# Kernel optimization log

Measured on AMD Instinct MI355X. Metric: run time of the kernel, lower is better.

## Reference

```python
import jax, jax.numpy as jnp
import numpy as np

N_NODES = 10000
N_EDGES = 160000
C = 16        # num_feature_channels
C2 = 8        # output channels per irrep per head (C/2)
HID = 64      # radial_network_hidden_units
NH = 2        # num_attention_heads
NG = 16       # graphs in batch
F_IN = 64     # num_features
F_OUT = 32    # number_of_output_features
HEAD_TYPES = ("normal", "inverse")  # invariant_dictionary
IRREP_SLICES = ((0, 1), (1, 4), (4, 9))  # l=0,1,2 blocks of the SH dim


def _sph_harm(r):
    """Component-normalized real spherical harmonics l=0..2 for unit vectors r [E,3] -> [E,9]."""
    x, y, z = r[:, 0], r[:, 1], r[:, 2]
    c3 = 1.7320508   # sqrt(3)
    c15 = 3.8729833  # sqrt(15)
    l0 = jnp.ones_like(x)[:, None]
    l1 = c3 * r
    l2 = jnp.stack([
        c15 * x * y,
        c15 * y * z,
        1.1180340 * (2.0 * z * z - x * x - y * y),  # sqrt(5)/2
        c15 * x * z,
        1.9364917 * (x * x - y * y),                 # sqrt(15)/2
    ], axis=-1)
    return jnp.concatenate([l0, l1, l2], axis=-1)


def setup_inputs() -> dict:
    key = jax.random.key(0)
    ks = jax.random.split(key, 16)
    node_features = jax.random.normal(ks[0], (N_NODES, F_IN), jnp.float32)
    pos = jax.random.normal(ks[1], (N_NODES, 3), jnp.float32)
    src = jax.random.randint(ks[2], (N_EDGES,), 0, N_NODES)
    off = jax.random.randint(ks[3], (N_EDGES,), 1, N_NODES)  # avoid self-loops (d=0)
    tgt = (src + off) % N_NODES
    edge_index = jnp.stack([src, tgt], axis=0)
    batch = jnp.sort(jax.random.randint(ks[4], (N_NODES,), 0, NG))
    s = lambda k, shape, fan: (jax.random.normal(k, shape, jnp.float32) / np.sqrt(fan)).astype(jnp.float32)
    return dict(
        node_features=node_features, pos=pos,
        W_embed=s(ks[5], (F_IN, C), F_IN), b_embed=jnp.zeros((C,), jnp.float32),
        Wq=s(ks[6], (NH, C, C), C), Wk=s(ks[7], (NH, C, C), C),
        W1=s(ks[8], (NH, 1, HID), 1), b1=jnp.zeros((NH, HID), jnp.float32),
        Wa=s(ks[9], (NH, HID), HID), Wv=s(ks[10], (NH, HID, C * 3), HID),
        Wo=s(ks[11], (NH, 3, C, C2), C),
        Wproj=s(ks[12], (NH * C2, F_OUT), NH * C2), bproj=jnp.zeros((F_OUT,), jnp.float32),
        edge_index=edge_index, batch=batch,
    )


def _forward(node_features, pos, W_embed, b_embed, Wq, Wk, W1, b1, Wa, Wv, Wo,
             Wproj, bproj, edge_index, batch):
    src, tgt = edge_index[0], edge_index[1]
    rel = pos[tgt] - pos[src]                       # [E,3]
    dist = jnp.linalg.norm(rel, axis=-1, keepdims=True)  # [E,1]
    rhat = rel / dist
    Y = _sph_harm(rhat)                             # [E,9]
    x = node_features @ W_embed + b_embed          # [N,C] scalar (0e) features
    xs = x[src]                                     # [E,C]
    inv_sqrt_c = 1.0 / np.sqrt(C)
    head_outs = []
    for h in range(NH):
        d_feat = dist if HEAD_TYPES[h] == "normal" else dist ** -2  # [E,1]
        hid = jax.nn.relu(d_feat @ W1[h] + b1[h])   # [E,HID] radial network
        att_bias = hid @ Wa[h]                      # [E]
        wv = (hid @ Wv[h]).reshape(-1, C, 3)        # [E,C,3] per-(channel,l) radial weights
        q = x @ Wq[h]
        k = x @ Wk[h]
        logit = jnp.sum(q[tgt] * k[src], axis=-1) * inv_sqrt_c + att_bias  # [E]
        # segment softmax over incoming edges of each target node
        m = jax.ops.segment_max(logit, tgt, num_segments=N_NODES)
        e = jnp.exp(logit - m[tgt])
        z = jax.ops.segment_sum(e, tgt, num_segments=N_NODES)
        alpha = e / z[tgt]                          # [E]
        # expand per-l weights to per-m: dims (1,3,5)
        wv_m = jnp.repeat(wv, np.array([1, 3, 5]), axis=2, total_repeat_length=9)  # [E,C,9]
        msg = (alpha[:, None, None] * wv_m) * xs[:, :, None] * Y[:, None, :]       # [E,C,9]
        node_out = jax.ops.segment_sum(msg, tgt, num_segments=N_NODES)             # [N,C,9]
        parts = [jnp.einsum('ncm,co->nom', node_out[:, :, s0:s1], Wo[h, li]).reshape(N_NODES, -1)
                 for li, (s0, s1) in enumerate(IRREP_SLICES)]
        head_outs.append(jnp.concatenate(parts, axis=-1))  # [N, C2*9]
    feat = jnp.concatenate(head_outs, axis=-1)              # [N, NH*C2*9]
    pooled = jax.ops.segment_sum(feat, batch, num_segments=NG)  # [NG, NH*C2*9]
    # equivariant Linear -> F_OUT x 0e: only scalar (l=0) components map to scalars
    blk = C2 * 9
    scal = jnp.concatenate([pooled[:, h * blk: h * blk + C2] for h in range(NH)], axis=-1)  # [NG, NH*C2]
    return scal @ Wproj + bproj                             # [NG, F_OUT]


def reference(node_features, pos, W_embed, b_embed, Wq, Wk, W1, b1, Wa, Wv, Wo,
              Wproj, bproj, edge_index, batch):
    return _forward(node_features, pos, W_embed, b_embed, Wq, Wk, W1, b1, Wa, Wv,
                    Wo, Wproj, bproj, edge_index, batch)
```

## Files before the change

### kernel.cpp

```cpp
#include <hip/hip_runtime.h>
#include <math.h>

#define NN 10000
#define NE 160000
#define CAP 96

__device__ __forceinline__ unsigned bf16pack2(float a, float b) {
    unsigned ua = __float_as_uint(a);
    unsigned ub = __float_as_uint(b);
    ua = ua + 0x7fffu + ((ua >> 16) & 1u);
    ub = ub + 0x7fffu + ((ub >> 16) & 1u);
    return (ua >> 16) | (ub & 0xffff0000u);
}

__global__ __launch_bounds__(256) void k_xqk(const float* __restrict__ nf,
        const float* __restrict__ We, const float* __restrict__ be,
        const float* __restrict__ Wq, const float* __restrict__ Wk,
        float* __restrict__ x, float* __restrict__ q, float* __restrict__ k,
        int* __restrict__ zeroReg) {
    int t = threadIdx.x;
    int gid = blockIdx.x * 256 + t;
    if (gid < 10256) zeroReg[gid] = 0;
    __shared__ float sWe[64 * 16];
    __shared__ float sWq[2 * 16 * 16];
    __shared__ float sWk[2 * 16 * 16];
    __shared__ float sNF[16 * 64];
    __shared__ float sX[16 * 16];
    for (int i = t; i < 1024; i += 256) sWe[i] = We[i];
    for (int i = t; i < 512; i += 256) { sWq[i] = Wq[i]; sWk[i] = Wk[i]; }
    int nodeBase = blockIdx.x * 16;
    for (int i = t; i < 1024; i += 256) {
        int n = nodeBase + (i >> 6);
        sNF[i] = (n < NN) ? nf[n * 64 + (i & 63)] : 0.0f;
    }
    __syncthreads();
    int ln = t >> 4, c = t & 15;
    int n = nodeBase + ln;
    float acc = be[c];
    #pragma unroll 16
    for (int j = 0; j < 64; ++j) acc = fmaf(sNF[ln * 64 + j], sWe[j * 16 + c], acc);
    sX[ln * 16 + c] = acc;
    __syncthreads();
    if (n < NN) {
        x[n * 16 + c] = acc;
        #pragma unroll
        for (int h = 0; h < 2; ++h) {
            float aq = 0.0f, ak = 0.0f;
            #pragma unroll
            for (int j = 0; j < 16; ++j) {
                float xv = sX[ln * 16 + j];
                aq = fmaf(xv, sWq[(h * 16 + j) * 16 + c], aq);
                ak = fmaf(xv, sWk[(h * 16 + j) * 16 + c], ak);
            }
            q[(n * 2 + h) * 16 + c] = aq;
            k[(n * 2 + h) * 16 + c] = ak;
        }
    }
}

__global__ __launch_bounds__(256) void k_prep(const float* __restrict__ W1,
        const float* __restrict__ b1, const float* __restrict__ Wa,
        const float* __restrict__ Wv,
        float* __restrict__ sTau, float* __restrict__ gT) {
    __shared__ float sW[128], sB[128], sA[128], sT[128];
    __shared__ float sV[2048];
    __shared__ int sRank[128];
    int t = threadIdx.x;
    if (t < 128) { sW[t] = W1[t]; sB[t] = b1[t]; sA[t] = Wa[t]; }
    for (int i = t; i < 2048; i += 256) {
        int h = i >> 10, j = (i >> 4) & 63, c = i & 15;
        sV[i] = Wv[(h * 64 + j) * 48 + 3 * c];
    }
    __syncthreads();
    if (t < 128) {
        float w = sW[t], b = sB[t];
        sT[t] = (w != 0.0f) ? (-b / w) : ((b > 0.0f) ? -INFINITY : INFINITY);
    }
    __syncthreads();
    if (t < 128) {
        int h = t >> 6, j = t & 63;
        float tau = sT[t];
        int r = 0;
        for (int jj = 0; jj < 64; ++jj) {
            float o = sT[h * 64 + jj];
            r += (o < tau) || (o == tau && jj < j);
        }
        sRank[t] = r;
        if (blockIdx.x == 0) sTau[h * 64 + r] = tau;
    }
    __syncthreads();
    int idx = blockIdx.x * 256 + t;
    if (idx < 2210) {
        int h = idx / 1105;
        int rem = idx - h * 1105;
        int k = rem / 17;
        int c = rem - k * 17;
        float A = 0.0f, B = 0.0f;
        for (int j = 0; j < 64; ++j) {
            int jj = h * 64 + j;
            float w = sW[jj], b = sB[jj];
            bool posSlope = (w >= 0.0f);
            int r = sRank[jj];
            bool active = posSlope ? (r < k) : (r >= k);
            if (active) {
                float v = (c < 16) ? sV[h * 1024 + j * 16 + c] : sA[jj];
                A = fmaf(w, v, A);
                B = fmaf(b, v, B);
            }
        }
        float* row = gT + (h * 65 + k) * 36;
        if (c < 16) { row[c] = A; row[20 + c] = B; }
        else        { row[16] = A; row[17] = B; }
    }
}

__global__ __launch_bounds__(256) void k_edge(const float* __restrict__ pos,
        const int* __restrict__ ei,
        const float* __restrict__ q, const float* __restrict__ k,
        const float* __restrict__ sTau, const float* __restrict__ gT,
        const float* __restrict__ Wo,
        const float* __restrict__ x, int* __restrict__ deg,
        float* __restrict__ lgp, uint4* __restrict__ gb) {
    int e = blockIdx.x * 256 + threadIdx.x;
    if (e >= NE) return;
    int s = ei[e], t = ei[NE + e];
    int p = atomicAdd(&deg[t], 1);
    bool ok = (p < CAP);
    size_t slot = (size_t)t * CAP + p;
    float dx = pos[t * 3 + 0] - pos[s * 3 + 0];
    float dy = pos[t * 3 + 1] - pos[s * 3 + 1];
    float dz = pos[t * 3 + 2] - pos[s * 3 + 2];
    float d = sqrtf(dx * dx + dy * dy + dz * dz);
    float fh[2] = { d, 1.0f / (d * d) };
    const float4* xp = (const float4*)(x + (size_t)s * 16);
    float4 xs0 = xp[0], xs1 = xp[1], xs2 = xp[2], xs3 = xp[3];
    float xf[16] = { xs0.x, xs0.y, xs0.z, xs0.w, xs1.x, xs1.y, xs1.z, xs1.w,
                     xs2.x, xs2.y, xs2.z, xs2.w, xs3.x, xs3.y, xs3.z, xs3.w };
    float L2v[2];
    #pragma unroll
    for (int h = 0; h < 2; ++h) {
        const float4* qt = (const float4*)(q + (size_t)t * 32 + h * 16);
        const float4* ks = (const float4*)(k + (size_t)s * 32 + h * 16);
        float4 a0 = qt[0], a1 = qt[1], a2 = qt[2], a3 = qt[3];
        float4 b0 = ks[0], c1 = ks[1], c2 = ks[2], c3 = ks[3];
        float dot = a0.x * b0.x + a0.y * b0.y + a0.z * b0.z + a0.w * b0.w
                  + a1.x * c1.x + a1.y * c1.y + a1.z * c1.z + a1.w * c1.w
                  + a2.x * c2.x + a2.y * c2.y + a2.z * c2.z + a2.w * c2.w
                  + a3.x * c3.x + a3.y * c3.y + a3.z * c3.z + a3.w * c3.w;
        float f = fh[h];
        const float* tb = sTau + h * 64;
        int kk = 0;
        #pragma unroll
        for (int step = 64; step >= 1; step >>= 1) {
            int mid = kk + step;
            if (mid <= 64 && tb[mid - 1] <= f) kk = mid;
        }
        const float* row = gT + (h * 65 + kk) * 36;
        float4 A0 = *(const float4*)(row + 0);
        float4 A1 = *(const float4*)(row + 4);
        float4 A2 = *(const float4*)(row + 8);
        float4 A3 = *(const float4*)(row + 12);
        float2 AB = *(const float2*)(row + 16);
        float4 B0 = *(const float4*)(row + 20);
        float4 B1 = *(const float4*)(row + 24);
        float4 B2 = *(const float4*)(row + 28);
        float4 B3 = *(const float4*)(row + 32);
        L2v[h] = fmaf(dot, 0.25f, fmaf(AB.x, f, AB.y));
        float acc[16] = {
            fmaf(A0.x, f, B0.x), fmaf(A0.y, f, B0.y), fmaf(A0.z, f, B0.z), fmaf(A0.w, f, B0.w),
            fmaf(A1.x, f, B1.x), fmaf(A1.y, f, B1.y), fmaf(A1.z, f, B1.z), fmaf(A1.w, f, B1.w),
            fmaf(A2.x, f, B2.x), fmaf(A2.y, f, B2.y), fmaf(A2.z, f, B2.z), fmaf(A2.w, f, B2.w),
            fmaf(A3.x, f, B3.x), fmaf(A3.y, f, B3.y), fmaf(A3.z, f, B3.z), fmaf(A3.w, f, B3.w) };
        float g[8] = {0,0,0,0,0,0,0,0};
        const float* wob = Wo + h * 384;
        #pragma unroll
        for (int c = 0; c < 16; ++c) {
            float axc = acc[c] * xf[c];
            #pragma unroll
            for (int o = 0; o < 8; ++o) g[o] = fmaf(axc, wob[c * 8 + o], g[o]);
        }
        if (ok) {
            gb[slot * 2 + h] = make_uint4(bf16pack2(g[0], g[1]), bf16pack2(g[2], g[3]),
                                          bf16pack2(g[4], g[5]), bf16pack2(g[6], g[7]));
        }
    }
    if (ok) *(float2*)(lgp + slot * 2) = make_float2(L2v[0], L2v[1]);
}

__global__ __launch_bounds__(256) void k_gather(const int* __restrict__ deg,
        const float* __restrict__ lgp, const unsigned* __restrict__ gb,
        float* __restrict__ feat) {
    int t0 = threadIdx.x;
    int wv = t0 >> 6;
    int lane = t0 & 63;
    int pid = blockIdx.x * 4 + wv;
    int n = pid >> 1, h = pid & 1;
    int dg = min(deg[n], CAP);
    int g = lane >> 2, p = lane & 3;
    float m = -INFINITY, z = 0.0f, u0 = 0.0f, u1 = 0.0f;
    const float* lgb = lgp + (size_t)n * (CAP * 2) + h;
    const unsigned* gbb = gb + (size_t)n * (CAP * 8) + h * 4 + p;
    for (int i = g; i < dg; i += 16) {
        float L = lgb[i * 2];
        unsigned wbits = gbb[(size_t)i * 8];
        float ga = __uint_as_float(wbits << 16);
        float gbv = __uint_as_float(wbits & 0xffff0000u);
        float nm = fmaxf(m, L);
        float sc = (m > -INFINITY) ? __expf(m - nm) : 0.0f;
        float w  = __expf(L - nm);
        u0 = fmaf(u0, sc, w * ga);
        u1 = fmaf(u1, sc, w * gbv);
        z  = fmaf(z, sc, w);
        m = nm;
    }
    #pragma unroll
    for (int off = 4; off <= 32; off <<= 1) {
        float mo = __shfl_xor(m, off, 64);
        float zo = __shfl_xor(z, off, 64);
        float a0o = __shfl_xor(u0, off, 64);
        float a1o = __shfl_xor(u1, off, 64);
        float nm = fmaxf(m, mo);
        float a = (m  > -INFINITY) ? __expf(m  - nm) : 0.0f;
        float b = (mo > -INFINITY) ? __expf(mo - nm) : 0.0f;
        u0 = u0 * a + a0o * b;
        u1 = u1 * a + a1o * b;
        z  = z * a + zo * b;
        m = nm;
    }
    if (lane < 4) {
        float inv = (z > 0.0f) ? 1.0f / z : 0.0f;
        *(float2*)(feat + n * 16 + h * 8 + p * 2) = make_float2(u0 * inv, u1 * inv);
    }
}

__global__ __launch_bounds__(256) void k_pool(const float* __restrict__ feat,
        const int* __restrict__ batch, float* __restrict__ pooled) {
    __shared__ float sP[256];
    int t = threadIdx.x;
    sP[t] = 0.0f;
    __syncthreads();
    int tid = blockIdx.x * 256 + t;
    int c = tid & 15, seg = tid >> 4;
    int n0 = seg * 16, n1 = min(n0 + 16, NN);
    float run = 0.0f;
    int curg = -1;
    for (int n = n0; n < n1; ++n) {
        int gg = batch[n];
        if (gg != curg) {
            if (curg >= 0) atomicAdd(&sP[curg * 16 + c], run);
            run = 0.0f; curg = gg;
        }
        run += feat[n * 16 + c];
    }
    if (curg >= 0) atomicAdd(&sP[curg * 16 + c], run);
    __syncthreads();
    atomicAdd(&pooled[t], sP[t]);
}

__global__ __launch_bounds__(512) void k_final(const float* __restrict__ pooled,
        const float* __restrict__ Wproj, const float* __restrict__ bproj,
        float* __restrict__ out) {
    int t = threadIdx.x;
    int g = t >> 5, fo = t & 31;
    float acc = bproj[fo];
    #pragma unroll
    for (int j = 0; j < 16; ++j) acc = fmaf(pooled[g * 16 + j], Wproj[j * 32 + fo], acc);
    out[g * 32 + fo] = acc;
}

extern "C" void kernel_launch(void* const* d_in, const int* in_sizes, int n_in,
                              void* d_out, int out_size, void* d_ws, size_t ws_size,
                              hipStream_t stream) {
    const float* nf    = (const float*)d_in[0];
    const float* pos   = (const float*)d_in[1];
    const float* We    = (const float*)d_in[2];
    const float* be    = (const float*)d_in[3];
    const float* Wq    = (const float*)d_in[4];
    const float* Wk    = (const float*)d_in[5];
    const float* W1    = (const float*)d_in[6];
    const float* b1    = (const float*)d_in[7];
    const float* Wa    = (const float*)d_in[8];
    const float* Wv    = (const float*)d_in[9];
    const float* Wo    = (const float*)d_in[10];
    const float* Wproj = (const float*)d_in[11];
    const float* bproj = (const float*)d_in[12];
    const int*   ei    = (const int*)d_in[13];
    const int*   batch = (const int*)d_in[14];
    float* out = (float*)d_out;
    (void)in_sizes; (void)n_in; (void)out_size; (void)ws_size;

    float* ws     = (float*)d_ws;
    float* x      = ws;
    float* q      = x + 160000;
    float* k      = q + 320000;
    float* feat   = k + 320000;
    float* pooled = feat + 160000;
    int*   deg    = (int*)(pooled + 256);
    float* sTau   = (float*)(deg + 10000);
    float* gT     = sTau + 128;
    float* lgp    = gT + 4680;
    unsigned* gbu = (unsigned*)(lgp + (size_t)NN * CAP * 2);

    hipLaunchKernelGGL(k_xqk,    dim3(625),  dim3(256), 0, stream, nf, We, be, Wq, Wk, x, q, k, (int*)pooled);
    hipLaunchKernelGGL(k_prep,   dim3(9),    dim3(256), 0, stream, W1, b1, Wa, Wv, sTau, gT);
    hipLaunchKernelGGL(k_edge,   dim3(625),  dim3(256), 0, stream, pos, ei, q, k, sTau, gT, Wo, x, deg, lgp, (uint4*)gbu);
    hipLaunchKernelGGL(k_gather, dim3(5000), dim3(256), 0, stream, deg, lgp, gbu, feat);
    hipLaunchKernelGGL(k_pool,   dim3(40),   dim3(256), 0, stream, feat, batch, pooled);
    hipLaunchKernelGGL(k_final,  dim3(1),    dim3(512), 0, stream, pooled, Wproj, bproj, out);
}
```

Baseline: 136.5 us.

## Fuse prep into xqk and gather/pool/final into one kernel with atomic tickets

Runs the radial-table prep as extra blocks of the node-embedding kernel, and merges gather, pooling and the final projection into one kernel. The last 40 blocks to finish (by atomic ticket) spin until all blocks are done, then pool, and the very last block computes the output. This cuts six launches to three, removing launch gaps and inter-kernel idle time. The cost is a spin-wait and device-scope fences, which depend on the ticketed blocks being resident while earlier blocks finish.

Result: slower. 520.9 us (+281.6%).

```diff
diff --git a/kernel.cpp b/kernel.cpp
--- a/kernel.cpp
+++ b/kernel.cpp
@@ -16,11 +16,66 @@
 __global__ __launch_bounds__(256) void k_xqk(const float* __restrict__ nf,
         const float* __restrict__ We, const float* __restrict__ be,
         const float* __restrict__ Wq, const float* __restrict__ Wk,
+        const float* __restrict__ W1, const float* __restrict__ b1,
+        const float* __restrict__ Wa, const float* __restrict__ Wv,
         float* __restrict__ x, float* __restrict__ q, float* __restrict__ k,
-        int* __restrict__ zeroReg) {
+        int* __restrict__ zeroReg, float* __restrict__ sTau, float* __restrict__ gT) {
     int t = threadIdx.x;
+    if (blockIdx.x >= 625) {
+        int pb = blockIdx.x - 625;
+        __shared__ float sW[128], sB[128], sA[128], sT[128];
+        __shared__ float sV[2048];
+        __shared__ int sRank[128];
+        if (t < 128) { sW[t] = W1[t]; sB[t] = b1[t]; sA[t] = Wa[t]; }
+        for (int i = t; i < 2048; i += 256) {
+            int h = i >> 10, j = (i >> 4) & 63, c = i & 15;
+            sV[i] = Wv[(h * 64 + j) * 48 + 3 * c];
+        }
+        __syncthreads();
+        if (t < 128) {
+            float w = sW[t], b = sB[t];
+            sT[t] = (w != 0.0f) ? (-b / w) : ((b > 0.0f) ? -INFINITY : INFINITY);
+        }
+        __syncthreads();
+        if (t < 128) {
+            int h = t >> 6, j = t & 63;
+            float tau = sT[t];
+            int r = 0;
+            for (int jj = 0; jj < 64; ++jj) {
+                float o = sT[h * 64 + jj];
+                r += (o < tau) || (o == tau && jj < j);
+            }
+            sRank[t] = r;
+            if (pb == 0) sTau[h * 64 + r] = tau;
+        }
+        __syncthreads();
+        int idx = pb * 256 + t;
+        if (idx < 2210) {
+            int h = idx / 1105;
+            int rem = idx - h * 1105;
+            int kk = rem / 17;
+            int c = rem - kk * 17;
+            float A = 0.0f, B = 0.0f;
+            for (int j = 0; j < 64; ++j) {
+                int jj = h * 64 + j;
+                float w = sW[jj], b = sB[jj];
+                bool posSlope = (w >= 0.0f);
+                int r = sRank[jj];
+                bool active = posSlope ? (r < kk) : (r >= kk);
+                if (active) {
+                    float v = (c < 16) ? sV[h * 1024 + j * 16 + c] : sA[jj];
+                    A = fmaf(w, v, A);
+                    B = fmaf(b, v, B);
+                }
+            }
+            float* row = gT + (h * 65 + kk) * 36;
+            if (c < 16) { row[c] = A; row[20 + c] = B; }
+            else        { row[16] = A; row[17] = B; }
+        }
+        return;
+    }
     int gid = blockIdx.x * 256 + t;
-    if (gid < 10256) zeroReg[gid] = 0;
+    if (gid < 10264) zeroReg[gid] = 0;
     __shared__ float sWe[64 * 16];
     __shared__ float sWq[2 * 16 * 16];
     __shared__ float sWk[2 * 16 * 16];
@@ -55,62 +110,6 @@
             q[(n * 2 + h) * 16 + c] = aq;
             k[(n * 2 + h) * 16 + c] = ak;
         }
-    }
-}
-
-__global__ __launch_bounds__(256) void k_prep(const float* __restrict__ W1,
-        const float* __restrict__ b1, const float* __restrict__ Wa,
-        const float* __restrict__ Wv,
-        float* __restrict__ sTau, float* __restrict__ gT) {
-    __shared__ float sW[128], sB[128], sA[128], sT[128];
-    __shared__ float sV[2048];
-    __shared__ int sRank[128];
-    int t = threadIdx.x;
-    if (t < 128) { sW[t] = W1[t]; sB[t] = b1[t]; sA[t] = Wa[t]; }
-    for (int i = t; i < 2048; i += 256) {
-        int h = i >> 10, j = (i >> 4) & 63, c = i & 15;
-        sV[i] = Wv[(h * 64 + j) * 48 + 3 * c];
-    }
-    __syncthreads();
-    if (t < 128) {
-        float w = sW[t], b = sB[t];
-        sT[t] = (w != 0.0f) ? (-b / w) : ((b > 0.0f) ? -INFINITY : INFINITY);
-    }
-    __syncthreads();
-    if (t < 128) {
-        int h = t >> 6, j = t & 63;
-        float tau = sT[t];
-        int r = 0;
-        for (int jj = 0; jj < 64; ++jj) {
-            float o = sT[h * 64 + jj];
-            r += (o < tau) || (o == tau && jj < j);
-        }
-        sRank[t] = r;
-        if (blockIdx.x == 0) sTau[h * 64 + r] = tau;
-    }
-    __syncthreads();
-    int idx = blockIdx.x * 256 + t;
-    if (idx < 2210) {
-        int h = idx / 1105;
-        int rem = idx - h * 1105;
-        int k = rem / 17;
-        int c = rem - k * 17;
-        float A = 0.0f, B = 0.0f;
-        for (int j = 0; j < 64; ++j) {
-            int jj = h * 64 + j;
-            float w = sW[jj], b = sB[jj];
-            bool posSlope = (w >= 0.0f);
-            int r = sRank[jj];
-            bool active = posSlope ? (r < k) : (r >= k);
-            if (active) {
-                float v = (c < 16) ? sV[h * 1024 + j * 16 + c] : sA[jj];
-                A = fmaf(w, v, A);
-                B = fmaf(b, v, B);
-            }
-        }
-        float* row = gT + (h * 65 + k) * 36;
-        if (c < 16) { row[c] = A; row[20 + c] = B; }
-        else        { row[16] = A; row[17] = B; }
     }
 }
 
@@ -187,85 +186,109 @@
     if (ok) *(float2*)(lgp + slot * 2) = make_float2(L2v[0], L2v[1]);
 }
 
-__global__ __launch_bounds__(256) void k_gather(const int* __restrict__ deg,
+__global__ __launch_bounds__(256) void k_gpf(const int* __restrict__ deg,
         const float* __restrict__ lgp, const unsigned* __restrict__ gb,
-        float* __restrict__ feat) {
+        const int* __restrict__ batch,
+        const float* __restrict__ Wproj, const float* __restrict__ bproj,
+        float* __restrict__ feat, float* __restrict__ pooled,
+        int* __restrict__ ctrs, float* __restrict__ out) {
+    __shared__ int sTicket;
+    __shared__ float sP[256];
+    __shared__ float sPool[256];
     int t0 = threadIdx.x;
-    int wv = t0 >> 6;
-    int lane = t0 & 63;
-    int pid = blockIdx.x * 4 + wv;
-    int n = pid >> 1, h = pid & 1;
-    int dg = min(deg[n], CAP);
-    int g = lane >> 2, p = lane & 3;
-    float m = -INFINITY, z = 0.0f, u0 = 0.0f, u1 = 0.0f;
-    const float* lgb = lgp + (size_t)n * (CAP * 2) + h;
-    const unsigned* gbb = gb + (size_t)n * (CAP * 8) + h * 4 + p;
-    for (int i = g; i < dg; i += 16) {
-        float L = lgb[i * 2];
-        unsigned wbits = gbb[(size_t)i * 8];
-        float ga = __uint_as_float(wbits << 16);
-        float gbv = __uint_as_float(wbits & 0xffff0000u);
-        float nm = fmaxf(m, L);
-        float sc = (m > -INFINITY) ? __expf(m - nm) : 0.0f;
-        float w  = __expf(L - nm);
-        u0 = fmaf(u0, sc, w * ga);
-        u1 = fmaf(u1, sc, w * gbv);
-        z  = fmaf(z, sc, w);
-        m = nm;
-    }
+    {
+        int wv = t0 >> 6;
+        int lane = t0 & 63;
+        int pid = blockIdx.x * 4 + wv;
+        int n = pid >> 1, h = pid & 1;
+        int dg = min(deg[n], CAP);
+        int g = lane >> 2, p = lane & 3;
+        float m = -INFINITY, z = 0.0f, u0 = 0.0f, u1 = 0.0f;
+        const float* lgb = lgp + (size_t)n * (CAP * 2) + h;
+        const unsigned* gbb = gb + (size_t)n * (CAP * 8) + h * 4 + p;
+        for (int i = g; i < dg; i += 16) {
+            float L = lgb[i * 2];
+            unsigned wbits = gbb[(size_t)i * 8];
+            float ga = __uint_as_float(wbits << 16);
+            float gbv = __uint_as_float(wbits & 0xffff0000u);
+            float nm = fmaxf(m, L);
+            float sc = (m > -INFINITY) ? __expf(m - nm) : 0.0f;
+            float w  = __expf(L - nm);
+            u0 = fmaf(u0, sc, w * ga);
+            u1 = fmaf(u1, sc, w * gbv);
+            z  = fmaf(z, sc, w);
+            m = nm;
+        }
+        #pragma unroll
+        for (int off = 4; off <= 32; off <<= 1) {
+            float mo = __shfl_xor(m, off, 64);
+            float zo = __shfl_xor(z, off, 64);
+            float a0o = __shfl_xor(u0, off, 64);
+            float a1o = __shfl_xor(u1, off, 64);
+            float nm = fmaxf(m, mo);
+            float a = (m  > -INFINITY) ? __expf(m  - nm) : 0.0f;
+            float b = (mo > -INFINITY) ? __expf(mo - nm) : 0.0f;
+            u0 = u0 * a + a0o * b;
+            u1 = u1 * a + a1o * b;
+            z  = z * a + zo * b;
+            m = nm;
+        }
+        if (lane < 4) {
+            float inv = (z > 0.0f) ? 1.0f / z : 0.0f;
+            *(float2*)(feat + n * 16 + h * 8 + p * 2) = make_float2(u0 * inv, u1 * inv);
+        }
+    }
+    __syncthreads();
+    __threadfence();
+    if (t0 == 0)
+        sTicket = __hip_atomic_fetch_add(&ctrs[0], 1, __ATOMIC_ACQ_REL, __HIP_MEMORY_SCOPE_AGENT);
+    __syncthreads();
+    int ticket = sTicket;
+    if (ticket < 4960) return;
+    int seg40 = ticket - 4960;
+    if (t0 == 0) {
+        while (__hip_atomic_load(&ctrs[0], __ATOMIC_ACQUIRE, __HIP_MEMORY_SCOPE_AGENT) < 5000)
+            __builtin_amdgcn_s_sleep(2);
+    }
+    __syncthreads();
+    __threadfence();
+    sP[t0] = 0.0f;
+    __syncthreads();
+    {
+        int tid = seg40 * 256 + t0;
+        int c = tid & 15, seg = tid >> 4;
+        int n0 = seg * 16, n1 = min(n0 + 16, NN);
+        float run = 0.0f;
+        int curg = -1;
+        for (int n = n0; n < n1; ++n) {
+            int gg = batch[n];
+            if (gg != curg) {
+                if (curg >= 0) atomicAdd(&sP[curg * 16 + c], run);
+                run = 0.0f; curg = gg;
+            }
+            run += feat[n * 16 + c];
+        }
+        if (curg >= 0) atomicAdd(&sP[curg * 16 + c], run);
+    }
+    __syncthreads();
+    atomicAdd(&pooled[t0], sP[t0]);
+    __threadfence();
+    if (t0 == 0)
+        sTicket = __hip_atomic_fetch_add(&ctrs[1], 1, __ATOMIC_ACQ_REL, __HIP_MEMORY_SCOPE_AGENT);
+    __syncthreads();
+    if (sTicket != 39) return;
+    __threadfence();
+    sPool[t0] = __hip_atomic_load(&pooled[t0], __ATOMIC_RELAXED, __HIP_MEMORY_SCOPE_AGENT);
+    __syncthreads();
     #pragma unroll
-    for (int off = 4; off <= 32; off <<= 1) {
-        float mo = __shfl_xor(m, off, 64);
-        float zo = __shfl_xor(z, off, 64);
-        float a0o = __shfl_xor(u0, off, 64);
-        float a1o = __shfl_xor(u1, off, 64);
-        float nm = fmaxf(m, mo);
-        float a = (m  > -INFINITY) ? __expf(m  - nm) : 0.0f;
-        float b = (mo > -INFINITY) ? __expf(mo - nm) : 0.0f;
-        u0 = u0 * a + a0o * b;
-        u1 = u1 * a + a1o * b;
-        z  = z * a + zo * b;
-        m = nm;
-    }
-    if (lane < 4) {
-        float inv = (z > 0.0f) ? 1.0f / z : 0.0f;
-        *(float2*)(feat + n * 16 + h * 8 + p * 2) = make_float2(u0 * inv, u1 * inv);
-    }
-}
-
-__global__ __launch_bounds__(256) void k_pool(const float* __restrict__ feat,
-        const int* __restrict__ batch, float* __restrict__ pooled) {
-    __shared__ float sP[256];
-    int t = threadIdx.x;
-    sP[t] = 0.0f;
-    __syncthreads();
-    int tid = blockIdx.x * 256 + t;
-    int c = tid & 15, seg = tid >> 4;
-    int n0 = seg * 16, n1 = min(n0 + 16, NN);
-    float run = 0.0f;
-    int curg = -1;
-    for (int n = n0; n < n1; ++n) {
-        int gg = batch[n];
-        if (gg != curg) {
-            if (curg >= 0) atomicAdd(&sP[curg * 16 + c], run);
-            run = 0.0f; curg = gg;
-        }
-        run += feat[n * 16 + c];
-    }
-    if (curg >= 0) atomicAdd(&sP[curg * 16 + c], run);
-    __syncthreads();
-    atomicAdd(&pooled[t], sP[t]);
-}
-
-__global__ __launch_bounds__(512) void k_final(const float* __restrict__ pooled,
-        const float* __restrict__ Wproj, const float* __restrict__ bproj,
-        float* __restrict__ out) {
-    int t = threadIdx.x;
-    int g = t >> 5, fo = t & 31;
-    float acc = bproj[fo];
-    #pragma unroll
-    for (int j = 0; j < 16; ++j) acc = fmaf(pooled[g * 16 + j], Wproj[j * 32 + fo], acc);
-    out[g * 32 + fo] = acc;
+    for (int r = 0; r < 2; ++r) {
+        int o = t0 + r * 256;
+        int g = o >> 5, fo = o & 31;
+        float acc = bproj[fo];
+        #pragma unroll
+        for (int j = 0; j < 16; ++j) acc = fmaf(sPool[g * 16 + j], Wproj[j * 32 + fo], acc);
+        out[o] = acc;
+    }
 }
 
 extern "C" void kernel_launch(void* const* d_in, const int* in_sizes, int n_in,
@@ -296,15 +319,16 @@
     float* feat   = k + 320000;
     float* pooled = feat + 160000;
     int*   deg    = (int*)(pooled + 256);
-    float* sTau   = (float*)(deg + 10000);
+    int*   ctrs   = deg + 10000;
+    float* sTau   = (float*)(ctrs + 8);
     float* gT     = sTau + 128;
     float* lgp    = gT + 4680;
     unsigned* gbu = (unsigned*)(lgp + (size_t)NN * CAP * 2);
 
-    hipLaunchKernelGGL(k_xqk,    dim3(625),  dim3(256), 0, stream, nf, We, be, Wq, Wk, x, q, k, (int*)pooled);
-    hipLaunchKernelGGL(k_prep,   dim3(9),    dim3(256), 0, stream, W1, b1, Wa, Wv, sTau, gT);
-    hipLaunchKernelGGL(k_edge,   dim3(625),  dim3(256), 0, stream, pos, ei, q, k, sTau, gT, Wo, x, deg, lgp, (uint4*)gbu);
-    hipLaunchKernelGGL(k_gather, dim3(5000), dim3(256), 0, stream, deg, lgp, gbu, feat);
-    hipLaunchKernelGGL(k_pool,   dim3(40),   dim3(256), 0, stream, feat, batch, pooled);
-    hipLaunchKernelGGL(k_final,  dim3(1),    dim3(512), 0, stream, pooled, Wproj, bproj, out);
-}
+    hipLaunchKernelGGL(k_xqk,  dim3(634),  dim3(256), 0, stream,
+                       nf, We, be, Wq, Wk, W1, b1, Wa, Wv, x, q, k, (int*)pooled, sTau, gT);
+    hipLaunchKernelGGL(k_edge, dim3(625),  dim3(256), 0, stream,
+                       pos, ei, q, k, sTau, gT, Wo, x, deg, lgp, (uint4*)gbu);
+    hipLaunchKernelGGL(k_gpf,  dim3(5000), dim3(256), 0, stream,
+                       deg, lgp, gbu, batch, Wproj, bproj, feat, pooled, ctrs, out);
+}
```
